# Performance work log

Measured on AMD Instinct MI355X. Metric: run time of the kernel, lower is better.

The kernel has to match this reference:

```python
import jax, jax.numpy as jnp
import numpy as np

KNN = 4
H = 0.03


def setup_inputs() -> dict:
    key = jax.random.key(0)
    pc = jax.random.normal(key, (8, 4096, 3), dtype=jnp.float32)  # [B, N, 3]
    return {"pc": pc}


def reference(pc) -> jnp.ndarray:
    sq = jnp.sum(pc * pc, axis=-1)  # [B, N]
    # dist[b, i, j] = || pc[b,i] - pc[b,j] ||^2
    dist = sq[:, :, None] + sq[:, None, :] - 2.0 * jnp.einsum("bid,bjd->bij", pc, pc)
    dist = jnp.maximum(dist, 0.0)
    # k nearest neighbors with offset=1 (skip self): take smallest KNN+1, drop the first
    neg_top, _ = jax.lax.top_k(-dist, KNN + 1)  # sorted descending -> distances ascending
    knn_dist = -neg_top[..., 1:]  # [B, N, KNN]
    weight = jnp.exp(-knn_dist / (H * H))
    loss = jnp.sum(-knn_dist * weight)
    return loss
```

## Files before the change

kernel.cpp:

```cpp
#include <hip/hip_runtime.h>
#include <math.h>

#define NPTS   4096
#define NB     8
#define TILE   64
#define NWAVES 8
#define BLK    (NWAVES * 64)
#define JCHUNK (NPTS / NWAVES)
#define INV_H2 (1.0f / (0.03f * 0.03f))

__device__ __forceinline__ float med3f(float a, float b, float c) {
#if defined(__has_builtin)
#if __has_builtin(__builtin_amdgcn_fmed3f)
  return __builtin_amdgcn_fmed3f(a, b, c);
#else
  return fminf(c, fmaxf(a, b));
#endif
#else
  return fminf(c, fmaxf(a, b));
#endif
}

template <bool CHECK>
__device__ __forceinline__ void scan_range(const float4* __restrict__ sP,
                                           int lo, int hi, int self,
                                           float mx, float my, float mz, float sqi,
                                           float& t0, float& t1, float& t2, float& t3) {
#pragma unroll 8
  for (int j = lo; j < hi; ++j) {
    float4 q = sP[j];
    float t = fmaf(mz, q.z, q.w);
    t = fmaf(my, q.y, t);
    t = fmaf(mx, q.x, t);
    float d = t + sqi;
    if (CHECK) d = (j == self) ? 3.0e38f : d;
    t3 = med3f(t2, d, t3);
    t2 = med3f(t1, d, t2);
    t1 = med3f(t0, d, t1);
    t0 = fminf(t0, d);
  }
}

__device__ __forceinline__ void merge4(float a0, float a1, float a2, float a3,
                                       float b0, float b1, float b2, float b3,
                                       float& o0, float& o1, float& o2, float& o3) {
  float L0 = fminf(a0, b3), L1 = fminf(a1, b2), L2 = fminf(a2, b1), L3 = fminf(a3, b0);
  float e0 = fminf(L0, L2), e2 = fmaxf(L0, L2);
  float e1 = fminf(L1, L3), e3 = fmaxf(L1, L3);
  o0 = fminf(e0, e1); o1 = fmaxf(e0, e1);
  o2 = fminf(e2, e3); o3 = fmaxf(e2, e3);
}

__global__ __launch_bounds__(BLK)
void repulsion_kernel(const float* __restrict__ pc, float* __restrict__ out) {
  __shared__ float4 sP[NPTS];
  __shared__ float4 cand4[NWAVES * TILE];

  const int blk  = blockIdx.x;
  const int b    = blk >> 6;
  const int tile = blk & 63;
  const int tid  = threadIdx.x;
  const float* base = pc + (size_t)b * NPTS * 3;
  const float4* pcv = (const float4*)base;

  for (int g = tid; g < NPTS / 4; g += BLK) {
    float4 a = pcv[3 * g + 0];
    float4 c = pcv[3 * g + 1];
    float4 e = pcv[3 * g + 2];
    float x0 = a.x, y0 = a.y, z0 = a.z;
    float x1 = a.w, y1 = c.x, z1 = c.y;
    float x2 = c.z, y2 = c.w, z2 = e.x;
    float x3 = e.y, y3 = e.z, z3 = e.w;
    sP[4 * g + 0] = make_float4(x0, y0, z0, fmaf(x0, x0, fmaf(y0, y0, z0 * z0)));
    sP[4 * g + 1] = make_float4(x1, y1, z1, fmaf(x1, x1, fmaf(y1, y1, z1 * z1)));
    sP[4 * g + 2] = make_float4(x2, y2, z2, fmaf(x2, x2, fmaf(y2, y2, z2 * z2)));
    sP[4 * g + 3] = make_float4(x3, y3, z3, fmaf(x3, x3, fmaf(y3, y3, z3 * z3)));
  }
  __syncthreads();

  const int w    = tid >> 6;
  const int lane = tid & 63;
  const int self = tile * TILE + lane;

  float4 me = sP[self];
  const float mx = -2.0f * me.x, my = -2.0f * me.y, mz = -2.0f * me.z;
  const float sqi = me.w;

  const float INF = 3.0e38f;
  float t0 = INF, t1 = INF, t2 = INF, t3 = INF;

  const int j0 = w * JCHUNK;
  const int selfwave = tile >> 3;
  if (w == selfwave) {
    const int s0 = tile * TILE;
    scan_range<false>(sP, j0, s0, self, mx, my, mz, sqi, t0, t1, t2, t3);
    scan_range<true >(sP, s0, s0 + TILE, self, mx, my, mz, sqi, t0, t1, t2, t3);
    scan_range<false>(sP, s0 + TILE, j0 + JCHUNK, self, mx, my, mz, sqi, t0, t1, t2, t3);
  } else {
    scan_range<false>(sP, j0, j0 + JCHUNK, self, mx, my, mz, sqi, t0, t1, t2, t3);
  }

  cand4[w * TILE + lane] = make_float4(t0, t1, t2, t3);
  __syncthreads();

  if (tid < 64) {
    float4 A = cand4[0 * TILE + lane];
    float4 B = cand4[1 * TILE + lane];
    float4 C = cand4[2 * TILE + lane];
    float4 D = cand4[3 * TILE + lane];
    float4 E = cand4[4 * TILE + lane];
    float4 F = cand4[5 * TILE + lane];
    float4 G = cand4[6 * TILE + lane];
    float4 H4 = cand4[7 * TILE + lane];
    float ab0, ab1, ab2, ab3, cd0, cd1, cd2, cd3;
    float ef0, ef1, ef2, ef3, gh0, gh1, gh2, gh3;
    merge4(A.x, A.y, A.z, A.w, B.x, B.y, B.z, B.w, ab0, ab1, ab2, ab3);
    merge4(C.x, C.y, C.z, C.w, D.x, D.y, D.z, D.w, cd0, cd1, cd2, cd3);
    merge4(E.x, E.y, E.z, E.w, F.x, F.y, F.z, F.w, ef0, ef1, ef2, ef3);
    merge4(G.x, G.y, G.z, G.w, H4.x, H4.y, H4.z, H4.w, gh0, gh1, gh2, gh3);
    float u0, u1, u2, u3, v0, v1, v2, v3;
    merge4(ab0, ab1, ab2, ab3, cd0, cd1, cd2, cd3, u0, u1, u2, u3);
    merge4(ef0, ef1, ef2, ef3, gh0, gh1, gh2, gh3, v0, v1, v2, v3);
    float m0 = fminf(u0, v3);
    float m1 = fminf(u1, v2);
    float m2 = fminf(u2, v1);
    float m3 = fminf(u3, v0);

    float s = 0.0f;
    s -= m0 * expf(-m0 * INV_H2);
    s -= m1 * expf(-m1 * INV_H2);
    s -= m2 * expf(-m2 * INV_H2);
    s -= m3 * expf(-m3 * INV_H2);

    for (int off = 32; off > 0; off >>= 1) s += __shfl_down(s, off);
    if (lane == 0) atomicAdd(out, s);
  }
}

extern "C" void kernel_launch(void* const* d_in, const int* in_sizes, int n_in,
                              void* d_out, int out_size, void* d_ws, size_t ws_size,
                              hipStream_t stream) {
  const float* pc = (const float*)d_in[0];
  float* out = (float*)d_out;
  hipMemsetAsync(out, 0, sizeof(float), stream);
  repulsion_kernel<<<dim3(NB * (NPTS / TILE)), dim3(BLK), 0, stream>>>(pc, out);
}
```

Before: 83.31 us.

## Process two query points per thread and enlarge tiles to 128 with 16 waves

Each thread now tracks top-4 lists for two query points, so every shared-memory load of a candidate point feeds two distance computations. The block grows to 16 waves with 128 queries per block, halving the grid and the per-block staging of the point cloud. The squared norm of the query is added and clamped at zero after the merge rather than inside the inner loop, and the final merge becomes a sequential loop over 16 partial lists. Register pressure doubles for the top-k state, and the larger 1024-thread blocks may reduce occupancy.

Result: no change. 82.22 us (-1.3%).

```diff
diff --git a/kernel.cpp b/kernel.cpp
--- a/kernel.cpp
+++ b/kernel.cpp
@@ -3,11 +3,12 @@
 
 #define NPTS   4096
 #define NB     8
-#define TILE   64
-#define NWAVES 8
+#define TILE   128
+#define NWAVES 16
 #define BLK    (NWAVES * 64)
 #define JCHUNK (NPTS / NWAVES)
 #define INV_H2 (1.0f / (0.03f * 0.03f))
+#define INFV   3.0e38f
 
 __device__ __forceinline__ float med3f(float a, float b, float c) {
 #if defined(__has_builtin)
@@ -21,23 +22,32 @@
 #endif
 }
 
-template <bool CHECK>
-__device__ __forceinline__ void scan_range(const float4* __restrict__ sP,
-                                           int lo, int hi, int self,
-                                           float mx, float my, float mz, float sqi,
-                                           float& t0, float& t1, float& t2, float& t3) {
+template <int CHECK>
+__device__ __forceinline__ void scan2(const float4* __restrict__ sP, int lo, int hi,
+                                      int self_lo, int self_hi,
+                                      float mxl, float myl, float mzl,
+                                      float mxh, float myh, float mzh,
+                                      float& a0, float& a1, float& a2, float& a3,
+                                      float& b0, float& b1, float& b2, float& b3) {
 #pragma unroll 8
   for (int j = lo; j < hi; ++j) {
     float4 q = sP[j];
-    float t = fmaf(mz, q.z, q.w);
-    t = fmaf(my, q.y, t);
-    t = fmaf(mx, q.x, t);
-    float d = t + sqi;
-    if (CHECK) d = (j == self) ? 3.0e38f : d;
-    t3 = med3f(t2, d, t3);
-    t2 = med3f(t1, d, t2);
-    t1 = med3f(t0, d, t1);
-    t0 = fminf(t0, d);
+    float tl = fmaf(mzl, q.z, q.w);
+    tl = fmaf(myl, q.y, tl);
+    tl = fmaf(mxl, q.x, tl);
+    float th = fmaf(mzh, q.z, q.w);
+    th = fmaf(myh, q.y, th);
+    th = fmaf(mxh, q.x, th);
+    if (CHECK == 1) tl = (j == self_lo) ? INFV : tl;
+    if (CHECK == 2) th = (j == self_hi) ? INFV : th;
+    a3 = med3f(a2, tl, a3);
+    a2 = med3f(a1, tl, a2);
+    a1 = med3f(a0, tl, a1);
+    a0 = fminf(a0, tl);
+    b3 = med3f(b2, th, b3);
+    b2 = med3f(b1, th, b2);
+    b1 = med3f(b0, th, b1);
+    b0 = fminf(b0, th);
   }
 }
 
@@ -54,16 +64,17 @@
 __global__ __launch_bounds__(BLK)
 void repulsion_kernel(const float* __restrict__ pc, float* __restrict__ out) {
   __shared__ float4 sP[NPTS];
-  __shared__ float4 cand4[NWAVES * TILE];
+  __shared__ float4 cand[NWAVES * TILE];
 
   const int blk  = blockIdx.x;
-  const int b    = blk >> 6;
-  const int tile = blk & 63;
+  const int b    = blk >> 5;
+  const int tile = blk & 31;
   const int tid  = threadIdx.x;
   const float* base = pc + (size_t)b * NPTS * 3;
   const float4* pcv = (const float4*)base;
 
-  for (int g = tid; g < NPTS / 4; g += BLK) {
+  {
+    const int g = tid;
     float4 a = pcv[3 * g + 0];
     float4 c = pcv[3 * g + 1];
     float4 e = pcv[3 * g + 2];
@@ -80,57 +91,58 @@
 
   const int w    = tid >> 6;
   const int lane = tid & 63;
-  const int self = tile * TILE + lane;
+  const int self_lo = tile * TILE + lane;
+  const int self_hi = self_lo + 64;
 
-  float4 me = sP[self];
-  const float mx = -2.0f * me.x, my = -2.0f * me.y, mz = -2.0f * me.z;
-  const float sqi = me.w;
+  float4 plo = sP[self_lo];
+  float4 phi = sP[self_hi];
+  const float mxl = -2.0f * plo.x, myl = -2.0f * plo.y, mzl = -2.0f * plo.z;
+  const float mxh = -2.0f * phi.x, myh = -2.0f * phi.y, mzh = -2.0f * phi.z;
 
-  const float INF = 3.0e38f;
-  float t0 = INF, t1 = INF, t2 = INF, t3 = INF;
+  float a0 = INFV, a1 = INFV, a2 = INFV, a3 = INFV;
+  float b0 = INFV, b1 = INFV, b2 = INFV, b3 = INFV;
 
   const int j0 = w * JCHUNK;
-  const int selfwave = tile >> 3;
-  if (w == selfwave) {
-    const int s0 = tile * TILE;
-    scan_range<false>(sP, j0, s0, self, mx, my, mz, sqi, t0, t1, t2, t3);
-    scan_range<true >(sP, s0, s0 + TILE, self, mx, my, mz, sqi, t0, t1, t2, t3);
-    scan_range<false>(sP, s0 + TILE, j0 + JCHUNK, self, mx, my, mz, sqi, t0, t1, t2, t3);
+  const int cs = tile >> 1;
+  if (w == cs) {
+    const int s = j0 + ((tile & 1) << 7);
+    scan2<0>(sP, j0, s, self_lo, self_hi, mxl, myl, mzl, mxh, myh, mzh,
+             a0, a1, a2, a3, b0, b1, b2, b3);
+    scan2<1>(sP, s, s + 64, self_lo, self_hi, mxl, myl, mzl, mxh, myh, mzh,
+             a0, a1, a2, a3, b0, b1, b2, b3);
+    scan2<2>(sP, s + 64, s + 128, self_lo, self_hi, mxl, myl, mzl, mxh, myh, mzh,
+             a0, a1, a2, a3, b0, b1, b2, b3);
+    scan2<0>(sP, s + 128, j0 + JCHUNK, self_lo, self_hi, mxl, myl, mzl, mxh, myh, mzh,
+             a0, a1, a2, a3, b0, b1, b2, b3);
   } else {
-    scan_range<false>(sP, j0, j0 + JCHUNK, self, mx, my, mz, sqi, t0, t1, t2, t3);
+    scan2<0>(sP, j0, j0 + JCHUNK, self_lo, self_hi, mxl, myl, mzl, mxh, myh, mzh,
+             a0, a1, a2, a3, b0, b1, b2, b3);
   }
 
-  cand4[w * TILE + lane] = make_float4(t0, t1, t2, t3);
+  cand[w * TILE + lane]      = make_float4(a0, a1, a2, a3);
+  cand[w * TILE + 64 + lane] = make_float4(b0, b1, b2, b3);
   __syncthreads();
 
-  if (tid < 64) {
-    float4 A = cand4[0 * TILE + lane];
-    float4 B = cand4[1 * TILE + lane];
-    float4 C = cand4[2 * TILE + lane];
-    float4 D = cand4[3 * TILE + lane];
-    float4 E = cand4[4 * TILE + lane];
-    float4 F = cand4[5 * TILE + lane];
-    float4 G = cand4[6 * TILE + lane];
-    float4 H4 = cand4[7 * TILE + lane];
-    float ab0, ab1, ab2, ab3, cd0, cd1, cd2, cd3;
-    float ef0, ef1, ef2, ef3, gh0, gh1, gh2, gh3;
-    merge4(A.x, A.y, A.z, A.w, B.x, B.y, B.z, B.w, ab0, ab1, ab2, ab3);
-    merge4(C.x, C.y, C.z, C.w, D.x, D.y, D.z, D.w, cd0, cd1, cd2, cd3);
-    merge4(E.x, E.y, E.z, E.w, F.x, F.y, F.z, F.w, ef0, ef1, ef2, ef3);
-    merge4(G.x, G.y, G.z, G.w, H4.x, H4.y, H4.z, H4.w, gh0, gh1, gh2, gh3);
-    float u0, u1, u2, u3, v0, v1, v2, v3;
-    merge4(ab0, ab1, ab2, ab3, cd0, cd1, cd2, cd3, u0, u1, u2, u3);
-    merge4(ef0, ef1, ef2, ef3, gh0, gh1, gh2, gh3, v0, v1, v2, v3);
-    float m0 = fminf(u0, v3);
-    float m1 = fminf(u1, v2);
-    float m2 = fminf(u2, v1);
-    float m3 = fminf(u3, v0);
+  if (tid < TILE) {
+    float4 M = cand[tid];
+    float m0 = M.x, m1 = M.y, m2 = M.z, m3 = M.w;
+#pragma unroll
+    for (int ww = 1; ww < NWAVES; ++ww) {
+      float4 Cw = cand[ww * TILE + tid];
+      merge4(m0, m1, m2, m3, Cw.x, Cw.y, Cw.z, Cw.w, m0, m1, m2, m3);
+    }
+
+    const float sqi = sP[tile * TILE + tid].w;
+    float d0 = fmaxf(m0 + sqi, 0.0f);
+    float d1 = fmaxf(m1 + sqi, 0.0f);
+    float d2 = fmaxf(m2 + sqi, 0.0f);
+    float d3 = fmaxf(m3 + sqi, 0.0f);
 
     float s = 0.0f;
-    s -= m0 * expf(-m0 * INV_H2);
-    s -= m1 * expf(-m1 * INV_H2);
-    s -= m2 * expf(-m2 * INV_H2);
-    s -= m3 * expf(-m3 * INV_H2);
+    s -= d0 * expf(-d0 * INV_H2);
+    s -= d1 * expf(-d1 * INV_H2);
+    s -= d2 * expf(-d2 * INV_H2);
+    s -= d3 * expf(-d3 * INV_H2);
 
     for (int off = 32; off > 0; off >>= 1) s += __shfl_down(s, off);
     if (lane == 0) atomicAdd(out, s);
```
